# Kernel tuning notes

Measured on AMD Instinct MI355X. Metric: run time of the kernel, lower is better.

The kernel has to match this reference:

```python
import jax, jax.numpy as jnp
import numpy as np

K_OUTLIER = 16  # decomposition_topk default k
Q = 127.0


def quantize(mat):
    # per-row symmetric int8 quantization (values kept in float, rounded)
    max_val = jnp.max(jnp.abs(mat), axis=-1)
    mat_q = jnp.round(mat * (Q / max_val)[..., None])
    return mat_q, max_val


def setup_inputs() -> dict:
    key = jax.random.key(0)
    kx, kw, kb = jax.random.split(key, 3)
    B, S, D_IN, D_OUT = 4, 2048, 4096, 4096
    x = jax.random.normal(kx, (B, S, D_IN), dtype=jnp.float32)
    W = jax.random.normal(kw, (D_OUT, D_IN), dtype=jnp.float32) * 0.02
    bias = jax.random.normal(kb, (D_OUT,), dtype=jnp.float32) * 0.02
    return {"x": x, "W": W, "bias": bias}


def reference(x, W, bias):
    # __init__: quantize weight once
    weight_q, w_max = quantize(W)  # [O, I], [O]

    # decomposition_topk: pick k columns with largest abs max over all rows
    col_max = jnp.max(jnp.abs(x.reshape(-1, x.shape[-1])), axis=0)  # [I]
    _, idx_unq = jax.lax.top_k(col_max, K_OUTLIER)  # [k]
    x_unq = x[..., idx_unq]                         # [B, S, k] outlier columns (fp)
    x_z = x.at[..., idx_unq].set(0.0)               # zero out outlier columns

    # quantize the non-outlier activations per row
    x_q, x_max = quantize(x_z)                      # [B, S, I], [B, S]

    # qlinear: simulated int8 GEMM done in fp32, then dequant via outer scale
    res_q = jnp.einsum('bsi,oi->bso', x_q, weight_q)  # [B, S, O]
    mx = x_max[..., None] * w_max                     # [B, S, O] outer of scales
    res = (res_q / (Q * Q)).astype(jnp.float16).astype(jnp.float32) * mx

    # outlier path in higher precision: dequantized weight columns
    weight_unq = weight_q[:, idx_unq] * w_max[:, None] / Q  # [O, k]
    res_unq = jnp.einsum('bsk,ok->bso', x_unq, weight_unq) + bias

    return res + res_unq
```

## Files before the change

kernel.cpp:

```cpp
#include <hip/hip_runtime.h>
#include <hip/hip_bf16.h>

#define NROWS 8192
#define DIN   4096
#define DOUT  4096
#define KOUT  16

typedef __attribute__((ext_vector_type(4)))  int  int4v;
typedef __attribute__((ext_vector_type(16))) int  int16v;

typedef const __attribute__((address_space(1))) void* gas1;
typedef __attribute__((address_space(3))) void* las3;

#define WS_COLMAX   0u
#define WS_MASK     16384u
#define WS_IDX      20480u
#define WS_WMAX     32768u
#define WS_XMAX     49152u
#define WS_WU       81920u
#define WS_XU       344064u
#define WS_WQ       1048576u
#define WS_XQ       34603008u

__global__ __launch_bounds__(256) void k_colmax(const float* __restrict__ x,
                                                unsigned int* __restrict__ colmax) {
  int col = blockIdx.x * 256 + threadIdx.x;
  size_t r0 = (size_t)blockIdx.y * 128;
  unsigned int m = 0;
  for (int r = 0; r < 128; ++r) {
    unsigned int b = __float_as_uint(x[(r0 + r) * DIN + col]) & 0x7fffffffu;
    m = b > m ? b : m;
  }
  atomicMax(&colmax[col], m);
}

__global__ __launch_bounds__(256) void k_topk(const unsigned int* __restrict__ colmax,
                                              int* __restrict__ idx,
                                              unsigned char* __restrict__ mask) {
  __shared__ unsigned long long keys[DIN];
  __shared__ unsigned long long red[256];
  int t = threadIdx.x;
  for (int i = t; i < DIN; i += 256) {
    keys[i] = (((unsigned long long)colmax[i]) << 12) | (unsigned long long)i;
    mask[i] = 0;
  }
  __syncthreads();
  for (int r = 0; r < KOUT; ++r) {
    unsigned long long m = 0;
    for (int i = t; i < DIN; i += 256) { unsigned long long k = keys[i]; m = k > m ? k : m; }
    red[t] = m;
    __syncthreads();
    for (int s = 128; s > 0; s >>= 1) {
      if (t < s) { unsigned long long o = red[t + s]; if (o > red[t]) red[t] = o; }
      __syncthreads();
    }
    if (t == 0) {
      int bi = (int)(red[0] & 0xFFFu);
      idx[r] = bi;
      mask[bi] = 1;
      keys[bi] = 0;
    }
    __syncthreads();
  }
}

__global__ __launch_bounds__(256) void k_quantW(const float* __restrict__ W,
                                                const int* __restrict__ idx,
                                                signed char* __restrict__ Wq,
                                                float* __restrict__ w_max,
                                                float* __restrict__ Wu) {
  __shared__ float row[DIN];
  __shared__ float red[256];
  int o = blockIdx.x, t = threadIdx.x;
  const float* Wr = W + (size_t)o * DIN;
  float m = 0.f;
  for (int i = t * 4; i < DIN; i += 1024) {
    float4 v = *(const float4*)(Wr + i);
    row[i+0] = v.x; row[i+1] = v.y; row[i+2] = v.z; row[i+3] = v.w;
    m = fmaxf(m, fmaxf(fmaxf(fabsf(v.x), fabsf(v.y)), fmaxf(fabsf(v.z), fabsf(v.w))));
  }
  red[t] = m;
  __syncthreads();
  for (int s = 128; s > 0; s >>= 1) {
    if (t < s) red[t] = fmaxf(red[t], red[t + s]);
    __syncthreads();
  }
  float mx = red[0];
  float sc = 127.0f / mx;
  signed char* Wqr = Wq + (size_t)o * DIN;
  for (int i = t * 4; i < DIN; i += 1024) {
    char4 q;
    q.x = (signed char)(int)rintf(row[i+0] * sc);
    q.y = (signed char)(int)rintf(row[i+1] * sc);
    q.z = (signed char)(int)rintf(row[i+2] * sc);
    q.w = (signed char)(int)rintf(row[i+3] * sc);
    *(char4*)(Wqr + i) = q;
  }
  if (t == 0) w_max[o] = mx;
  if (t < KOUT) {
    float wq = rintf(row[idx[t]] * sc);
    Wu[(size_t)o * KOUT + t] = wq * mx / 127.0f;
  }
}

__global__ __launch_bounds__(256) void k_quantX(const float* __restrict__ x,
                                                const unsigned char* __restrict__ mask,
                                                const int* __restrict__ idx,
                                                signed char* __restrict__ Xq,
                                                float* __restrict__ x_max,
                                                float* __restrict__ Xu) {
  __shared__ float row[DIN];
  __shared__ float red[256];
  int r = blockIdx.x, t = threadIdx.x;
  const float* xr = x + (size_t)r * DIN;
  float m = 0.f;
  for (int i = t * 4; i < DIN; i += 1024) {
    float4 v = *(const float4*)(xr + i);
    float a0 = mask[i+0] ? 0.f : v.x;
    float a1 = mask[i+1] ? 0.f : v.y;
    float a2 = mask[i+2] ? 0.f : v.z;
    float a3 = mask[i+3] ? 0.f : v.w;
    row[i+0] = a0; row[i+1] = a1; row[i+2] = a2; row[i+3] = a3;
    m = fmaxf(m, fmaxf(fmaxf(fabsf(a0), fabsf(a1)), fmaxf(fabsf(a2), fabsf(a3))));
  }
  red[t] = m;
  __syncthreads();
  for (int s = 128; s > 0; s >>= 1) {
    if (t < s) red[t] = fmaxf(red[t], red[t + s]);
    __syncthreads();
  }
  float mx = red[0];
  float sc = 127.0f / mx;
  signed char* Xqr = Xq + (size_t)r * DIN;
  for (int i = t * 4; i < DIN; i += 1024) {
    char4 q;
    q.x = (signed char)(int)rintf(row[i+0] * sc);
    q.y = (signed char)(int)rintf(row[i+1] * sc);
    q.z = (signed char)(int)rintf(row[i+2] * sc);
    q.w = (signed char)(int)rintf(row[i+3] * sc);
    *(char4*)(Xqr + i) = q;
  }
  if (t == 0) x_max[r] = mx;
  if (t < KOUT) Xu[(size_t)r * KOUT + t] = xr[idx[t]];
}

__global__ __launch_bounds__(512, 4) void k_gemm(const signed char* __restrict__ Xq,
                                                 const signed char* __restrict__ Wq,
                                                 const float* __restrict__ x_max,
                                                 const float* __restrict__ w_max,
                                                 const float* __restrict__ Xu,
                                                 const float* __restrict__ Wu,
                                                 const float* __restrict__ bias,
                                                 float* __restrict__ out) {
  __shared__ char smem[32768];
  signed char* sA = (signed char*)smem;
  signed char* sB = sA + 128 * 128;

  int t = threadIdx.x;
  int wid = t >> 6, l = t & 63;
  int wr = wid >> 2, wc = wid & 3;
  int l31 = l & 31, lh = l >> 5;
  int sw = l & 7;

  int bid = blockIdx.x;
  int wg = (bid & 7) * 256 + (bid >> 3);
  int bM = wg >> 5, bN = wg & 31;

  const signed char* Ab = Xq + (size_t)bM * 128 * DIN;
  const signed char* Bb = Wq + (size_t)bN * 128 * DIN;

  int16v acc[2];
  #pragma unroll
  for (int i = 0; i < 2; ++i)
    acc[i] = (int16v){0,0,0,0, 0,0,0,0, 0,0,0,0, 0,0,0,0};

  int srow = wid * 16 + (l >> 3);
  int skel = (((l & 7) ^ ((l >> 3) & 7)) * 16);

  for (int kt = 0; kt < DIN / 128; ++kt) {
    #pragma unroll
    for (int i = 0; i < 2; ++i) {
      int mrow = srow + i * 8;
      __builtin_amdgcn_global_load_lds((gas1)(Ab + (size_t)mrow * DIN + kt * 128 + skel),
                                       (las3)(sA + (wid * 16 + i * 8) * 128), 16, 0, 0);
      __builtin_amdgcn_global_load_lds((gas1)(Bb + (size_t)mrow * DIN + kt * 128 + skel),
                                       (las3)(sB + (wid * 16 + i * 8) * 128), 16, 0, 0);
    }
    __syncthreads();
    #pragma unroll
    for (int kk = 0; kk < 4; ++kk) {
      int c = (((kk * 2 + lh) ^ sw) * 16);
      int4v a0 = *(const int4v*)(sA + (wr * 64 + l31) * 128 + c);
      int4v a1 = *(const int4v*)(sA + (wr * 64 + 32 + l31) * 128 + c);
      int4v b0 = *(const int4v*)(sB + (wc * 32 + l31) * 128 + c);
      acc[0] = __builtin_amdgcn_mfma_i32_32x32x32_i8(a0, b0, acc[0], 0, 0, 0);
      acc[1] = __builtin_amdgcn_mfma_i32_32x32x32_i8(a1, b0, acc[1], 0, 0, 0);
    }
    __syncthreads();
  }

  float* eXu = (float*)smem;
  float* eWu = eXu + 128 * 17;
  float* exm = eWu + 128 * 17;
  float* ewm = exm + 128;
  float* ebs = ewm + 128;

  for (int i = t; i < 128 * KOUT; i += 512) {
    int rr = i >> 4, k = i & 15;
    eXu[rr * 17 + k] = Xu[((size_t)(bM * 128 + rr)) * KOUT + k];
    eWu[rr * 17 + k] = Wu[((size_t)(bN * 128 + rr)) * KOUT + k];
  }
  if (t < 128) {
    exm[t] = x_max[bM * 128 + t];
    ewm[t] = w_max[bN * 128 + t];
    ebs[t] = bias[bN * 128 + t];
  }
  __syncthreads();

  int cl = wc * 32 + l31;
  float wmc = ewm[cl];
  float bsc = ebs[cl];
  #pragma unroll
  for (int mi = 0; mi < 2; ++mi) {
    #pragma unroll
    for (int reg = 0; reg < 16; ++reg) {
      int rl = wr * 64 + mi * 32 + (reg & 3) + 8 * (reg >> 2) + 4 * lh;
      float xm = exm[rl];
      float rq = (float)acc[mi][reg];
      float v = (float)(_Float16)(rq / 16129.0f) * (xm * wmc);
      float dot = 0.f;
      #pragma unroll
      for (int k = 0; k < KOUT; ++k) dot = fmaf(eXu[rl * 17 + k], eWu[cl * 17 + k], dot);
      out[((size_t)(bM * 128 + rl)) * DOUT + (size_t)bN * 128 + cl] = v + dot + bsc;
    }
  }
}

extern "C" void kernel_launch(void* const* d_in, const int* in_sizes, int n_in,
                              void* d_out, int out_size, void* d_ws, size_t ws_size,
                              hipStream_t stream) {
  const float* x    = (const float*)d_in[0];
  const float* W    = (const float*)d_in[1];
  const float* bias = (const float*)d_in[2];
  float* out = (float*)d_out;
  char* ws = (char*)d_ws;

  unsigned int*   colmax = (unsigned int*)(ws + WS_COLMAX);
  unsigned char*  mask   = (unsigned char*)(ws + WS_MASK);
  int*            idx    = (int*)(ws + WS_IDX);
  float*          w_max  = (float*)(ws + WS_WMAX);
  float*          x_max  = (float*)(ws + WS_XMAX);
  float*          Wu     = (float*)(ws + WS_WU);
  float*          Xu     = (float*)(ws + WS_XU);
  signed char*    Wq     = (signed char*)(ws + WS_WQ);
  signed char*    Xq     = (signed char*)(ws + WS_XQ);

  hipMemsetAsync(colmax, 0, DIN * sizeof(unsigned int), stream);
  k_colmax<<<dim3(DIN / 256, NROWS / 128), 256, 0, stream>>>(x, colmax);
  k_topk<<<1, 256, 0, stream>>>(colmax, idx, mask);
  k_quantW<<<DOUT, 256, 0, stream>>>(W, idx, Wq, w_max, Wu);
  k_quantX<<<NROWS, 256, 0, stream>>>(x, mask, idx, Xq, x_max, Xu);
  k_gemm<<<2048, 512, 0, stream>>>(Xq, Wq, x_max, w_max, Xu, Wu, bias, out);
}
```

Measured before the change: 337.1 us.

## Double-buffer LDS tiles in int8 GEMM to overlap global loads with MFMA

```diff
diff --git a/kernel.cpp b/kernel.cpp
--- a/kernel.cpp
+++ b/kernel.cpp
@@ -5,6 +5,7 @@
 #define DIN   4096
 #define DOUT  4096
 #define KOUT  16
+#define NKT   (DIN / 128)
 
 typedef __attribute__((ext_vector_type(4)))  int  int4v;
 typedef __attribute__((ext_vector_type(16))) int  int16v;
@@ -152,9 +153,9 @@
                                                  const float* __restrict__ Wu,
                                                  const float* __restrict__ bias,
                                                  float* __restrict__ out) {
-  __shared__ char smem[32768];
+  __shared__ char smem[65536];
   signed char* sA = (signed char*)smem;
-  signed char* sB = sA + 128 * 128;
+  signed char* sB = sA + 2 * 128 * 128;
 
   int t = threadIdx.x;
   int wid = t >> 6, l = t & 63;
@@ -177,22 +178,31 @@
   int srow = wid * 16 + (l >> 3);
   int skel = (((l & 7) ^ ((l >> 3) & 7)) * 16);
 
-  for (int kt = 0; kt < DIN / 128; ++kt) {
-    #pragma unroll
-    for (int i = 0; i < 2; ++i) {
-      int mrow = srow + i * 8;
-      __builtin_amdgcn_global_load_lds((gas1)(Ab + (size_t)mrow * DIN + kt * 128 + skel),
-                                       (las3)(sA + (wid * 16 + i * 8) * 128), 16, 0, 0);
-      __builtin_amdgcn_global_load_lds((gas1)(Bb + (size_t)mrow * DIN + kt * 128 + skel),
-                                       (las3)(sB + (wid * 16 + i * 8) * 128), 16, 0, 0);
-    }
-    __syncthreads();
+#define STAGE(kt_, buf_) do { \
+  _Pragma("unroll") \
+  for (int i = 0; i < 2; ++i) { \
+    int mrow = srow + i * 8; \
+    __builtin_amdgcn_global_load_lds((gas1)(Ab + (size_t)mrow * DIN + (kt_) * 128 + skel), \
+                                     (las3)(sA + (buf_) * 16384 + (wid * 16 + i * 8) * 128), 16, 0, 0); \
+    __builtin_amdgcn_global_load_lds((gas1)(Bb + (size_t)mrow * DIN + (kt_) * 128 + skel), \
+                                     (las3)(sB + (buf_) * 16384 + (wid * 16 + i * 8) * 128), 16, 0, 0); \
+  } \
+} while (0)
+
+  STAGE(0, 0);
+  __syncthreads();
+
+  for (int kt = 0; kt < NKT; ++kt) {
+    int buf = kt & 1;
+    if (kt + 1 < NKT) STAGE(kt + 1, buf ^ 1);
+    const signed char* sAb = sA + buf * 16384;
+    const signed char* sBb = sB + buf * 16384;
     #pragma unroll
     for (int kk = 0; kk < 4; ++kk) {
       int c = (((kk * 2 + lh) ^ sw) * 16);
-      int4v a0 = *(const int4v*)(sA + (wr * 64 + l31) * 128 + c);
-      int4v a1 = *(const int4v*)(sA + (wr * 64 + 32 + l31) * 128 + c);
-      int4v b0 = *(const int4v*)(sB + (wc * 32 + l31) * 128 + c);
+      int4v a0 = *(const int4v*)(sAb + (wr * 64 + l31) * 128 + c);
+      int4v a1 = *(const int4v*)(sAb + (wr * 64 + 32 + l31) * 128 + c);
+      int4v b0 = *(const int4v*)(sBb + (wc * 32 + l31) * 128 + c);
       acc[0] = __builtin_amdgcn_mfma_i32_32x32x32_i8(a0, b0, acc[0], 0, 0, 0);
       acc[1] = __builtin_amdgcn_mfma_i32_32x32x32_i8(a1, b0, acc[1], 0, 0, 0);
     }
```

After: 331.6 us, median of 2. Within noise of the previous version (-1.6%).
